# Kernel tuning notes

Measured on AMD Instinct MI355X. Metric: run time of the kernel, lower is better.

Reference implementation:

```python
import jax, jax.numpy as jnp
import numpy as np

BS, C, H, W = 2, 128, 80, 160
P, G = 9, 8
GC = C // G
EPS = 1e-5


def _layernorm_c(x, g, b):
    # x: (bs, C, H, W); LayerNorm over channel dim (to_3d dim=2 -> norm over c)
    m = jnp.mean(x, axis=1, keepdims=True)
    v = jnp.mean((x - m) ** 2, axis=1, keepdims=True)
    return (x - m) / jnp.sqrt(v + EPS) * g[None, :, None, None] + b[None, :, None, None]


def _conv1x1(x, w, b):
    return jnp.einsum('bchw,oc->bohw', x, w) + b[None, :, None, None]


def _bilinear_sample(feat, pts):
    # feat (bs,C,H,W); pts (bs,N,2) normalized [0,1]; zero padding outside (DAF convention)
    bs, c, h, w = feat.shape
    x = pts[..., 0] * w - 0.5
    y = pts[..., 1] * h - 0.5
    x0 = jnp.floor(x)
    y0 = jnp.floor(y)
    dx = x - x0
    dy = y - y0
    x0i = x0.astype(jnp.int32)
    y0i = y0.astype(jnp.int32)

    def corner(xi, yi, wgt):
        valid = (xi >= 0) & (xi < w) & (yi >= 0) & (yi < h)
        xc = jnp.clip(xi, 0, w - 1)
        yc = jnp.clip(yi, 0, h - 1)
        g = jax.vmap(lambda f, yy, xx: f[:, yy, xx].T)(feat, yc, xc)  # (bs,N,C)
        return g * (wgt * valid)[..., None]

    return (corner(x0i, y0i, (1 - dx) * (1 - dy))
            + corner(x0i + 1, y0i, dx * (1 - dy))
            + corner(x0i, y0i + 1, (1 - dx) * dy)
            + corner(x0i + 1, y0i + 1, dx * dy))


def _branch(match_flat, anchor, feat_value, wmap, kp_w, kp_b):
    bs = feat_value.shape[0]
    hw = H * W
    # Sparse1DKeyPointsGenerator: learned 1D offsets along the disparity (x) direction
    off = match_flat @ kp_w.T + kp_b  # (bs, HW, P)
    anc = anchor.reshape(bs, hw, P, 2)
    kp = jnp.stack([anc[..., 0] + off, anc[..., 1]], axis=-1)  # (bs,HW,P,2)
    # group-softmax attention weights over num_pts
    wts = wmap.transpose(0, 2, 3, 1).reshape(bs, hw, P, G)  # channel c = p*G + g
    wts = jax.nn.softmax(wts, axis=2)
    # deformable aggregation: bilinear gather at key points + group-weighted sum over pts
    sampled = _bilinear_sample(feat_value, kp.reshape(bs, hw * P, 2))
    sampled = sampled.reshape(bs, hw, P, G, GC)
    out = jnp.einsum('bnpgc,bnpg->bngc', sampled, wts).reshape(bs, hw, C)
    out = out.reshape(bs, H, W, C).transpose(0, 3, 1, 2)
    return out, kp


def _forward(mask, match, context, geometric, context_anchor_points, geometric_anchor_points,
             ln_g, ln_b, lnc_g, lnc_b, lng_g, lng_b,
             wc_w, wc_b, wg_w, wg_b, vc_w, vc_b, vg_w, vg_b,
             out_w, out_b, kpc_w, kpc_b, kpg_w, kpg_b):
    bs = match.shape[0]
    hw = H * W
    match_n = _layernorm_c(match, ln_g, ln_b)
    context_n = _layernorm_c(context, lnc_g, lnc_b)
    geometric_n = _layernorm_c(geometric, lng_g, lng_b)
    ctx_val = _conv1x1(context_n, vc_w, vc_b)
    geo_val = _conv1x1(geometric_n, vg_w, vg_b)
    match_flat = match_n.reshape(bs, C, hw).transpose(0, 2, 1)  # (bs,HW,C)
    wc = _conv1x1(match_n, wc_w, wc_b)  # (bs,G*P,H,W)
    wg = _conv1x1(match_n, wg_w, wg_b)
    ctx_out, ctx_kp = _branch(match_flat, context_anchor_points, ctx_val, wc, kpc_w, kpc_b)
    geo_out, geo_kp = _branch(match_flat, geometric_anchor_points, geo_val, wg, kpg_w, kpg_b)
    out = jnp.concatenate([ctx_out * mask, geo_out], axis=1)
    out = _conv1x1(out, out_w, out_b)  # proj_drop is identity (p=0)
    return out, ctx_kp.reshape(bs, H, W, P, 2), geo_kp.reshape(bs, H, W, P, 2)


def setup_inputs() -> dict:
    key = jax.random.key(0)
    ks = jax.random.split(key, 20)

    def wn(k, shape):
        return jax.random.normal(k, shape, jnp.float32) * 0.02

    return {
        'mask': jax.random.uniform(ks[0], (BS, 1, H, W), jnp.float32),
        'match': jax.random.normal(ks[1], (BS, C, H, W), jnp.float32),
        'context': jax.random.normal(ks[2], (BS, C, H, W), jnp.float32),
        'geometric': jax.random.normal(ks[3], (BS, C, H, W), jnp.float32),
        'context_anchor_points': jax.random.uniform(ks[4], (BS, H, W, P, 2), jnp.float32),
        'geometric_anchor_points': jax.random.uniform(ks[5], (BS, H, W, P, 2), jnp.float32),
        'ln_g': jnp.ones((C,), jnp.float32), 'ln_b': jnp.zeros((C,), jnp.float32),
        'lnc_g': jnp.ones((C,), jnp.float32), 'lnc_b': jnp.zeros((C,), jnp.float32),
        'lng_g': jnp.ones((C,), jnp.float32), 'lng_b': jnp.zeros((C,), jnp.float32),
        'wc_w': wn(ks[6], (G * P, C)), 'wc_b': jnp.zeros((G * P,), jnp.float32),
        'wg_w': wn(ks[7], (G * P, C)), 'wg_b': jnp.zeros((G * P,), jnp.float32),
        'vc_w': wn(ks[8], (C, C)), 'vc_b': jnp.zeros((C,), jnp.float32),
        'vg_w': wn(ks[9], (C, C)), 'vg_b': jnp.zeros((C,), jnp.float32),
        'out_w': wn(ks[10], (C, 2 * C)), 'out_b': jnp.zeros((C,), jnp.float32),
        'kpc_w': wn(ks[11], (P, C)), 'kpc_b': jnp.zeros((P,), jnp.float32),
        'kpg_w': wn(ks[12], (P, C)), 'kpg_b': jnp.zeros((P,), jnp.float32),
    }


def reference(mask, match, context, geometric, context_anchor_points, geometric_anchor_points,
              ln_g, ln_b, lnc_g, lnc_b, lng_g, lng_b,
              wc_w, wc_b, wg_w, wg_b, vc_w, vc_b, vg_w, vg_b,
              out_w, out_b, kpc_w, kpc_b, kpg_w, kpg_b):
    return _forward(mask, match, context, geometric, context_anchor_points, geometric_anchor_points,
                    ln_g, ln_b, lnc_g, lnc_b, lng_g, lng_b,
                    wc_w, wc_b, wg_w, wg_b, vc_w, vc_b, vg_w, vg_b,
                    out_w, out_b, kpc_w, kpc_b, kpg_w, kpg_b)
```

## Files before the change

### kernel.cpp

```cpp
#include <hip/hip_runtime.h>
#include <hip/hip_bf16.h>

typedef __hip_bfloat16 bf16;
typedef __bf16 b16x8 __attribute__((ext_vector_type(8)));
typedef float f32x4 __attribute__((ext_vector_type(4)));
typedef float f32x2 __attribute__((ext_vector_type(2)));

#define HWs   12800
#define NPIX  25600
#define IMG_H 80
#define IMG_W 160

#define OFF_VCB  0
#define OFF_VGB  16384
#define OFF_MATB 32768
#define OFF_OUTB 53504
#define NW_BF16  86272

static __device__ inline unsigned char enc_fp8(float v)
{
    return (unsigned char)(__builtin_amdgcn_cvt_pk_fp8_f32(v, v, 0, false) & 0xFF);
}

__global__ __launch_bounds__(256) void k_prep(
    const float* __restrict__ vc_w, const float* __restrict__ vg_w,
    const float* __restrict__ wc_w, const float* __restrict__ wg_w,
    const float* __restrict__ kpc_w, const float* __restrict__ kpg_w,
    const float* __restrict__ out_w,
    const float* __restrict__ wc_b, const float* __restrict__ wg_b,
    const float* __restrict__ kpc_b, const float* __restrict__ kpg_b,
    bf16* __restrict__ wbuf, float* __restrict__ bias176)
{
    int i = blockIdx.x * 256 + threadIdx.x;
    if (i < 16384) {
        wbuf[i] = __float2bfloat16(vc_w[i]);
    } else if (i < 32768) {
        wbuf[i] = __float2bfloat16(vg_w[i - 16384]);
    } else if (i < 53504) {
        int j = i - 32768; int row = j >> 7; int c = j & 127;
        float v;
        if (row < 72)       v = wc_w[row * 128 + c];
        else if (row < 144) v = wg_w[(row - 72) * 128 + c];
        else if (row < 153) v = kpc_w[(row - 144) * 128 + c];
        else                v = kpg_w[(row - 153) * 128 + c];
        wbuf[i] = __float2bfloat16(v);
    } else if (i < NW_BF16) {
        wbuf[i] = __float2bfloat16(out_w[i - 53504]);
    } else if (i < NW_BF16 + 176) {
        int j = i - NW_BF16;
        float v = 0.f;
        if (j < 72)       v = wc_b[j];
        else if (j < 144) v = wg_b[j - 72];
        else if (j < 153) v = kpc_b[j - 144];
        else if (j < 162) v = kpg_b[j - 153];
        bias176[j] = v;
    }
}

__global__ __launch_bounds__(256) void k_stage1(
    const float* __restrict__ match, const float* __restrict__ context, const float* __restrict__ geometric,
    const float* __restrict__ ln_g, const float* __restrict__ ln_b,
    const float* __restrict__ lnc_g, const float* __restrict__ lnc_b,
    const float* __restrict__ lng_g, const float* __restrict__ lng_b,
    const float* __restrict__ vc_b, const float* __restrict__ vg_b,
    const bf16* __restrict__ wbuf, const float* __restrict__ bias176,
    const float* __restrict__ anc_c, const float* __restrict__ anc_g,
    unsigned char* __restrict__ ctx8, unsigned char* __restrict__ geo8,
    bf16* __restrict__ wts_g, float* __restrict__ coords_g,
    float* __restrict__ kp_out)
{
    __shared__ __align__(16) bf16 tile_s[32 * 136];
    __shared__ bf16 logit_s[32 * 144];
    __shared__ float offs_s[32 * 18];
    __shared__ float red1[8][32];
    __shared__ float red2[8][32];

    int bx = blockIdx.x;
    int seg = bx / 800;
    int tile = bx - seg * 800;
    int t = threadIdx.x;
    int pixbase = tile * 32;

    const float* X  = (seg == 0) ? context : (seg == 1) ? geometric : match;
    const float* gg = (seg == 0) ? lnc_g   : (seg == 1) ? lng_g     : ln_g;
    const float* bb = (seg == 0) ? lnc_b   : (seg == 1) ? lng_b     : ln_b;

    int p = t & 31;
    int cq = t >> 5;
    int b = pixbase >= HWs;
    int hw = pixbase - b * HWs;
    const float* base = X + ((size_t)b * 128) * HWs + hw + p;
    float xv[16];
#pragma unroll
    for (int j = 0; j < 16; j++) xv[j] = base[(size_t)(cq * 16 + j) * HWs];

    int wv = t >> 6;
    int lane = t & 63;
    int s = wv >> 1;
    int h = wv & 1;
    int lrow = lane & 15;
    int lq = lane >> 4;
    const bf16* Wb = (seg == 0) ? wbuf + OFF_VCB
                   : (seg == 1) ? wbuf + OFF_VGB
                                : wbuf + OFF_MATB;
    b16x8 wf[4][4];
    float bpre[4];
#pragma unroll
    for (int i = 0; i < 4; i++) {
        int o = (h + 2 * i) * 16 + lrow;
        const bf16* wr = Wb + (size_t)o * 128;
#pragma unroll
        for (int kk = 0; kk < 4; kk++)
            wf[i][kk] = *(const b16x8*)(wr + (kk * 4 + lq) * 8);
        bpre[i] = (seg == 0) ? vc_b[o] : (seg == 1) ? vg_b[o] : bias176[o];
    }

    {
        float s1 = 0.f, s2 = 0.f;
#pragma unroll
        for (int j = 0; j < 16; j++) { s1 += xv[j]; s2 += xv[j] * xv[j]; }
        red1[cq][p] = s1; red2[cq][p] = s2;
        __syncthreads();
        float S1 = 0.f, S2 = 0.f;
#pragma unroll
        for (int q = 0; q < 8; q++) { S1 += red1[q][p]; S2 += red2[q][p]; }
        float mean = S1 * (1.f / 128.f);
        float var  = fmaxf(S2 * (1.f / 128.f) - mean * mean, 0.f);
        float rstd = rsqrtf(var + 1e-5f);
#pragma unroll
        for (int j = 0; j < 16; j++) {
            int c = cq * 16 + j;
            float y = (xv[j] - mean) * rstd * gg[c] + bb[c];
            tile_s[p * 136 + c] = __float2bfloat16(y);
        }
        __syncthreads();
    }

    const b16x8* arow = (const b16x8*)(tile_s + (s * 16 + lrow) * 136);
    b16x8 af[4];
#pragma unroll
    for (int kk = 0; kk < 4; kk++) af[kk] = arow[kk * 4 + lq];

    if (seg < 2) {
        unsigned char* val = (seg == 0) ? ctx8 : geo8;
#pragma unroll
        for (int i = 0; i < 4; i++) {
            int o = (h + 2 * i) * 16 + lrow;
            f32x4 acc = {0.f, 0.f, 0.f, 0.f};
#pragma unroll
            for (int kk = 0; kk < 4; kk++)
                acc = __builtin_amdgcn_mfma_f32_16x16x32_bf16(af[kk], wf[i][kk], acc, 0, 0, 0);
#pragma unroll
            for (int r = 0; r < 4; r++) {
                int pix = pixbase + s * 16 + lq * 4 + r;
                val[(size_t)pix * 128 + o] = enc_fp8(acc[r] + bpre[i]);
            }
        }
        return;
    }

#pragma unroll
    for (int i = 0; i < 4; i++) {
        int o = (h + 2 * i) * 16 + lrow;
        f32x4 acc = {0.f, 0.f, 0.f, 0.f};
#pragma unroll
        for (int kk = 0; kk < 4; kk++)
            acc = __builtin_amdgcn_mfma_f32_16x16x32_bf16(af[kk], wf[i][kk], acc, 0, 0, 0);
#pragma unroll
        for (int r = 0; r < 4; r++) {
            int row = s * 16 + lq * 4 + r;
            logit_s[row * 144 + o] = __float2bfloat16(acc[r] + bpre[i]);
        }
    }
    for (int ot = h + 8; ot < 11; ot += 2) {
        int o = ot * 16 + lrow;
        const bf16* wr = Wb + (size_t)o * 128;
        f32x4 acc = {0.f, 0.f, 0.f, 0.f};
#pragma unroll
        for (int kk = 0; kk < 4; kk++)
            acc = __builtin_amdgcn_mfma_f32_16x16x32_bf16(af[kk], *(const b16x8*)(wr + (kk * 4 + lq) * 8), acc, 0, 0, 0);
        float bias = bias176[o];
#pragma unroll
        for (int r = 0; r < 4; r++) {
            int row = s * 16 + lq * 4 + r;
            float v = acc[r] + bias;
            if (o < 144)       logit_s[row * 144 + o] = __float2bfloat16(v);
            else if (o < 162)  offs_s[row * 18 + (o - 144)] = v;
        }
    }
    __syncthreads();

#pragma unroll
    for (int i = 0; i < 2; i++) {
        int task = t + 256 * i;
        int lp = task >> 4;
        int sub = task & 15;
        int br = sub >> 3;
        int g = sub & 7;
        const bf16* basel = logit_s + lp * 144 + br * 72 + g;
        float v[9];
        float m = -1e30f;
#pragma unroll
        for (int pp = 0; pp < 9; pp++) { v[pp] = __bfloat162float(basel[pp * 8]); m = fmaxf(m, v[pp]); }
        float ssum = 0.f;
#pragma unroll
        for (int pp = 0; pp < 9; pp++) { v[pp] = __expf(v[pp] - m); ssum += v[pp]; }
        float inv = 1.f / ssum;
        int pix = pixbase + lp;
        bf16* wbp = wts_g + ((size_t)pix * 2 + br) * 72 + g * 9;
#pragma unroll
        for (int pp = 0; pp < 9; pp++) wbp[pp] = __float2bfloat16(v[pp] * inv);
    }

    for (int i = 0; i < 3; i++) {
        int task = t + 256 * i;
        if (task < 576) {
            int lp = task / 18;
            int sub = task - lp * 18;
            int br = sub / 9;
            int pp = sub - br * 9;
            int pix = pixbase + lp;
            float off = offs_s[lp * 18 + br * 9 + pp];
            const float* anc = br ? anc_g : anc_c;
            float ax = anc[(size_t)pix * 18 + pp * 2];
            float ay = anc[(size_t)pix * 18 + pp * 2 + 1];
            float kx = ax + off;
            float* kpo = kp_out + (size_t)br * (NPIX * 18) + (size_t)pix * 18 + pp * 2;
            kpo[0] = kx;
            kpo[1] = ay;
            float* cbp = coords_g + ((size_t)pix * 2 + br) * 18 + pp * 2;
            cbp[0] = kx * 160.f - 0.5f;
            cbp[1] = ay * 80.f - 0.5f;
        }
    }
}

__global__ __launch_bounds__(256) void k_agg(
    const unsigned char* __restrict__ ctx8, const unsigned char* __restrict__ geo8,
    const bf16* __restrict__ wts_g, const float* __restrict__ coords_g,
    const float* __restrict__ mask,
    bf16* __restrict__ aggf)
{
    int t = threadIdx.x;
    int wv = t >> 6;
    int lane = t & 63;
    int q = lane >> 4;
    int sub = lane & 15;
    int c0 = sub * 8;
    int g = sub >> 1;

    int bx = blockIdx.x;
    int xcd = bx & 7;
    int br = xcd >> 2;
    int grp = (bx >> 3) * 4 + (xcd & 3);
    int pix = grp * 16 + wv * 4 + q;
    int tk = pix * 2 + br;
    int b = pix >= HWs;
    int rowbase = b * HWs;

    const unsigned char* val = br ? geo8 : ctx8;
    const float* cb = coords_g + (size_t)tk * 18;
    const bf16* wb = wts_g + (size_t)tk * 72 + g * 9;

    float wtv[9];
#pragma unroll
    for (int pp = 0; pp < 9; pp++) wtv[pp] = __bfloat162float(wb[pp]);

    float acc[8] = {0.f, 0.f, 0.f, 0.f, 0.f, 0.f, 0.f, 0.f};
    for (int pp = 0; pp < 9; pp++) {
        float px = cb[pp * 2];
        float py = cb[pp * 2 + 1];
        float fx = floorf(px), fy = floorf(py);
        float dx = px - fx, dy = py - fy;
        int x0 = (int)fx, y0 = (int)fy;
        float wt = wtv[pp];
#pragma unroll
        for (int c4 = 0; c4 < 4; c4++) {
            int xi = x0 + (c4 & 1);
            int yi = y0 + (c4 >> 1);
            bool ok = (xi >= 0) & (xi < IMG_W) & (yi >= 0) & (yi < IMG_H);
            int xc = min(max(xi, 0), IMG_W - 1);
            int yc = min(max(yi, 0), IMG_H - 1);
            float wx = (c4 & 1) ? dx : 1.f - dx;
            float wy = (c4 >> 1) ? dy : 1.f - dy;
            float wgt = ok ? wx * wy * wt : 0.f;
            uint2 u = *(const uint2*)(val + (size_t)(rowbase + yc * IMG_W + xc) * 128 + c0);
            f32x2 v01 = __builtin_amdgcn_cvt_pk_f32_fp8(u.x, false);
            f32x2 v23 = __builtin_amdgcn_cvt_pk_f32_fp8(u.x, true);
            f32x2 v45 = __builtin_amdgcn_cvt_pk_f32_fp8(u.y, false);
            f32x2 v67 = __builtin_amdgcn_cvt_pk_f32_fp8(u.y, true);
            acc[0] += wgt * v01[0]; acc[1] += wgt * v01[1];
            acc[2] += wgt * v23[0]; acc[3] += wgt * v23[1];
            acc[4] += wgt * v45[0]; acc[5] += wgt * v45[1];
            acc[6] += wgt * v67[0]; acc[7] += wgt * v67[1];
        }
    }
    float mv = (br == 0) ? mask[pix] : 1.f;
    b16x8 pk;
#pragma unroll
    for (int j = 0; j < 8; j++) pk[j] = (__bf16)(acc[j] * mv);
    *(b16x8*)(aggf + (size_t)pix * 256 + br * 128 + c0) = pk;
}

__global__ __launch_bounds__(256) void k_out(
    const bf16* __restrict__ aggf,
    const bf16* __restrict__ outb, const float* __restrict__ out_b,
    float* __restrict__ out)
{
    int t = threadIdx.x;
    int pixbase = blockIdx.x * 32;
    int wv = t >> 6;
    int lane = t & 63;
    int s = wv >> 1;
    int h = wv & 1;
    int lrow = lane & 15;
    int lq = lane >> 4;
    const b16x8* arow = (const b16x8*)(aggf + (size_t)(pixbase + s * 16 + lrow) * 256);
    b16x8 af[8];
#pragma unroll
    for (int kk = 0; kk < 8; kk++) af[kk] = arow[kk * 4 + lq];
    int b = pixbase >= HWs;
#pragma unroll
    for (int i = 0; i < 4; i++) {
        int o = (h + 2 * i) * 16 + lrow;
        const bf16* wrow = outb + (size_t)o * 256;
        f32x4 acc = {0.f, 0.f, 0.f, 0.f};
#pragma unroll
        for (int kk = 0; kk < 8; kk++)
            acc = __builtin_amdgcn_mfma_f32_16x16x32_bf16(af[kk], *(const b16x8*)(wrow + (kk * 4 + lq) * 8), acc, 0, 0, 0);
        float bias = out_b[o];
#pragma unroll
        for (int r = 0; r < 4; r++) {
            int pix = pixbase + s * 16 + lq * 4 + r;
            int hw = pix - b * HWs;
            out[(size_t)b * (128 * HWs) + (size_t)o * HWs + hw] = acc[r] + bias;
        }
    }
}

extern "C" void kernel_launch(void* const* d_in, const int* in_sizes, int n_in,
                              void* d_out, int out_size, void* d_ws, size_t ws_size,
                              hipStream_t stream)
{
    const float* mask      = (const float*)d_in[0];
    const float* match     = (const float*)d_in[1];
    const float* context   = (const float*)d_in[2];
    const float* geometric = (const float*)d_in[3];
    const float* anc_c     = (const float*)d_in[4];
    const float* anc_g     = (const float*)d_in[5];
    const float* ln_g  = (const float*)d_in[6];
    const float* ln_b  = (const float*)d_in[7];
    const float* lnc_g = (const float*)d_in[8];
    const float* lnc_b = (const float*)d_in[9];
    const float* lng_g = (const float*)d_in[10];
    const float* lng_b = (const float*)d_in[11];
    const float* wc_w  = (const float*)d_in[12];
    const float* wc_b  = (const float*)d_in[13];
    const float* wg_w  = (const float*)d_in[14];
    const float* wg_b  = (const float*)d_in[15];
    const float* vc_w  = (const float*)d_in[16];
    const float* vc_b  = (const float*)d_in[17];
    const float* vg_w  = (const float*)d_in[18];
    const float* vg_b  = (const float*)d_in[19];
    const float* out_w = (const float*)d_in[20];
    const float* out_b = (const float*)d_in[21];
    const float* kpc_w = (const float*)d_in[22];
    const float* kpc_b = (const float*)d_in[23];
    const float* kpg_w = (const float*)d_in[24];
    const float* kpg_b = (const float*)d_in[25];

    char* w = (char*)d_ws;
    unsigned char* ctx8 = (unsigned char*)(w);
    unsigned char* geo8 = (unsigned char*)(w + 3276800);
    bf16*  wts_g    = (bf16*)(w + 6553600);
    float* coords_g = (float*)(w + 13926400);
    bf16*  aggf     = (bf16*)(w + 17612800);
    bf16*  wbuf     = (bf16*)(w + 30720000);
    float* bias176  = (float*)(w + 30892544);

    float* outp = (float*)d_out;
    float* kp_out = outp + (size_t)2 * 128 * HWs;

    k_prep<<<(NW_BF16 + 176 + 255) / 256, 256, 0, stream>>>(
        vc_w, vg_w, wc_w, wg_w, kpc_w, kpg_w, out_w,
        wc_b, wg_b, kpc_b, kpg_b, wbuf, bias176);
    k_stage1<<<2400, 256, 0, stream>>>(match, context, geometric,
                                       ln_g, ln_b, lnc_g, lnc_b, lng_g, lng_b,
                                       vc_b, vg_b, wbuf, bias176,
                                       anc_c, anc_g,
                                       ctx8, geo8, wts_g, coords_g, kp_out);
    k_agg<<<3200, 256, 0, stream>>>(ctx8, geo8, wts_g, coords_g, mask, aggf);
    k_out<<<800, 256, 0, stream>>>(aggf, wbuf + OFF_OUTB, out_b, outp);
}
```

Baseline: 202.3 us.

## Fuse aggregation with output projection and transpose MFMA for vectorized stores

Merges the deformable aggregation and output 1x1 projection into one kernel so the aggregated features stay in shared memory instead of round-tripping through a global bf16 buffer, and drops one launch. Stage 1 swaps the MFMA operand order so each lane holds four consecutive output channels. This lets the fp8 value stores, bf16 logit stores and kp/coord writes become packed vector stores. It also interleaves segment assignment across blocks. In exchange, each fused block handles both branches for 16 pixels serially, which may lower parallelism in the gather phase.

```diff
diff --git a/kernel.cpp b/kernel.cpp
--- a/kernel.cpp
+++ b/kernel.cpp
@@ -3,6 +3,7 @@
 
 typedef __hip_bfloat16 bf16;
 typedef __bf16 b16x8 __attribute__((ext_vector_type(8)));
+typedef __bf16 b16x4 __attribute__((ext_vector_type(4)));
 typedef float f32x4 __attribute__((ext_vector_type(4)));
 typedef float f32x2 __attribute__((ext_vector_type(2)));
 
@@ -16,11 +17,6 @@
 #define OFF_MATB 32768
 #define OFF_OUTB 53504
 #define NW_BF16  86272
-
-static __device__ inline unsigned char enc_fp8(float v)
-{
-    return (unsigned char)(__builtin_amdgcn_cvt_pk_fp8_f32(v, v, 0, false) & 0xFF);
-}
 
 __global__ __launch_bounds__(256) void k_prep(
     const float* __restrict__ vc_w, const float* __restrict__ vg_w,
@@ -70,14 +66,14 @@
     float* __restrict__ kp_out)
 {
     __shared__ __align__(16) bf16 tile_s[32 * 136];
-    __shared__ bf16 logit_s[32 * 144];
+    __shared__ __align__(16) bf16 logit_s[32 * 148];
     __shared__ float offs_s[32 * 18];
     __shared__ float red1[8][32];
     __shared__ float red2[8][32];
 
     int bx = blockIdx.x;
-    int seg = bx / 800;
-    int tile = bx - seg * 800;
+    int seg = bx % 3;
+    int tile = bx / 3;
     int t = threadIdx.x;
     int pixbase = tile * 32;
 
@@ -104,7 +100,6 @@
                    : (seg == 1) ? wbuf + OFF_VGB
                                 : wbuf + OFF_MATB;
     b16x8 wf[4][4];
-    float bpre[4];
 #pragma unroll
     for (int i = 0; i < 4; i++) {
         int o = (h + 2 * i) * 16 + lrow;
@@ -112,7 +107,6 @@
 #pragma unroll
         for (int kk = 0; kk < 4; kk++)
             wf[i][kk] = *(const b16x8*)(wr + (kk * 4 + lq) * 8);
-        bpre[i] = (seg == 0) ? vc_b[o] : (seg == 1) ? vg_b[o] : bias176[o];
     }
 
     {
@@ -141,51 +135,62 @@
 #pragma unroll
     for (int kk = 0; kk < 4; kk++) af[kk] = arow[kk * 4 + lq];
 
+    int prow = s * 16 + lrow;
+
     if (seg < 2) {
         unsigned char* val = (seg == 0) ? ctx8 : geo8;
+        const float* vb = (seg == 0) ? vc_b : vg_b;
+        size_t prix = (size_t)(pixbase + prow) * 128;
 #pragma unroll
         for (int i = 0; i < 4; i++) {
-            int o = (h + 2 * i) * 16 + lrow;
+            int obase = (h + 2 * i) * 16 + lq * 4;
             f32x4 acc = {0.f, 0.f, 0.f, 0.f};
 #pragma unroll
             for (int kk = 0; kk < 4; kk++)
-                acc = __builtin_amdgcn_mfma_f32_16x16x32_bf16(af[kk], wf[i][kk], acc, 0, 0, 0);
-#pragma unroll
-            for (int r = 0; r < 4; r++) {
-                int pix = pixbase + s * 16 + lq * 4 + r;
-                val[(size_t)pix * 128 + o] = enc_fp8(acc[r] + bpre[i]);
+                acc = __builtin_amdgcn_mfma_f32_16x16x32_bf16(wf[i][kk], af[kk], acc, 0, 0, 0);
+            f32x4 bv = *(const f32x4*)(vb + obase);
+            int u = __builtin_amdgcn_cvt_pk_fp8_f32(acc[0] + bv[0], acc[1] + bv[1], 0, false);
+            u = __builtin_amdgcn_cvt_pk_fp8_f32(acc[2] + bv[2], acc[3] + bv[3], u, true);
+            *(unsigned int*)(val + prix + obase) = (unsigned int)u;
+        }
+        return;
+    }
+
+#pragma unroll
+    for (int i = 0; i < 4; i++) {
+        int obase = (h + 2 * i) * 16 + lq * 4;
+        f32x4 acc = {0.f, 0.f, 0.f, 0.f};
+#pragma unroll
+        for (int kk = 0; kk < 4; kk++)
+            acc = __builtin_amdgcn_mfma_f32_16x16x32_bf16(wf[i][kk], af[kk], acc, 0, 0, 0);
+        f32x4 bv = *(const f32x4*)(bias176 + obase);
+        b16x4 pk4;
+#pragma unroll
+        for (int r = 0; r < 4; r++) pk4[r] = (__bf16)(acc[r] + bv[r]);
+        *(b16x4*)(logit_s + prow * 148 + obase) = pk4;
+    }
+    for (int ot = h + 8; ot < 11; ot += 2) {
+        int obase = ot * 16 + lq * 4;
+        const bf16* wr = Wb + (size_t)(ot * 16 + lrow) * 128;
+        f32x4 acc = {0.f, 0.f, 0.f, 0.f};
+#pragma unroll
+        for (int kk = 0; kk < 4; kk++)
+            acc = __builtin_amdgcn_mfma_f32_16x16x32_bf16(*(const b16x8*)(wr + (kk * 4 + lq) * 8), af[kk], acc, 0, 0, 0);
+        f32x4 bv = *(const f32x4*)(bias176 + obase);
+        if (ot == 8) {
+            b16x4 pk4;
+#pragma unroll
+            for (int r = 0; r < 4; r++) pk4[r] = (__bf16)(acc[r] + bv[r]);
+            *(b16x4*)(logit_s + prow * 148 + obase) = pk4;
+        } else if (ot == 9) {
+#pragma unroll
+            for (int r = 0; r < 4; r++)
+                offs_s[prow * 18 + (obase - 144) + r] = acc[r] + bv[r];
+        } else {
+            if (lq == 0) {
+                offs_s[prow * 18 + 16] = acc[0] + bv[0];
+                offs_s[prow * 18 + 17] = acc[1] + bv[1];
             }
-        }
-        return;
-    }
-
-#pragma unroll
-    for (int i = 0; i < 4; i++) {
-        int o = (h + 2 * i) * 16 + lrow;
-        f32x4 acc = {0.f, 0.f, 0.f, 0.f};
-#pragma unroll
-        for (int kk = 0; kk < 4; kk++)
-            acc = __builtin_amdgcn_mfma_f32_16x16x32_bf16(af[kk], wf[i][kk], acc, 0, 0, 0);
-#pragma unroll
-        for (int r = 0; r < 4; r++) {
-            int row = s * 16 + lq * 4 + r;
-            logit_s[row * 144 + o] = __float2bfloat16(acc[r] + bpre[i]);
-        }
-    }
-    for (int ot = h + 8; ot < 11; ot += 2) {
-        int o = ot * 16 + lrow;
-        const bf16* wr = Wb + (size_t)o * 128;
-        f32x4 acc = {0.f, 0.f, 0.f, 0.f};
-#pragma unroll
-        for (int kk = 0; kk < 4; kk++)
-            acc = __builtin_amdgcn_mfma_f32_16x16x32_bf16(af[kk], *(const b16x8*)(wr + (kk * 4 + lq) * 8), acc, 0, 0, 0);
-        float bias = bias176[o];
-#pragma unroll
-        for (int r = 0; r < 4; r++) {
-            int row = s * 16 + lq * 4 + r;
-            float v = acc[r] + bias;
-            if (o < 144)       logit_s[row * 144 + o] = __float2bfloat16(v);
-            else if (o < 162)  offs_s[row * 18 + (o - 144)] = v;
         }
     }
     __syncthreads();
@@ -197,7 +202,7 @@
         int sub = task & 15;
         int br = sub >> 3;
         int g = sub & 7;
-        const bf16* basel = logit_s + lp * 144 + br * 72 + g;
+        const bf16* basel = logit_s + lp * 148 + br * 72 + g;
         float v[9];
         float m = -1e30f;
 #pragma unroll
@@ -216,31 +221,31 @@
         int task = t + 256 * i;
         if (task < 576) {
             int lp = task / 18;
-            int sub = task - lp * 18;
-            int br = sub / 9;
-            int pp = sub - br * 9;
+            int sub2 = task - lp * 18;
+            int br = sub2 / 9;
+            int pp = sub2 - br * 9;
             int pix = pixbase + lp;
             float off = offs_s[lp * 18 + br * 9 + pp];
             const float* anc = br ? anc_g : anc_c;
-            float ax = anc[(size_t)pix * 18 + pp * 2];
-            float ay = anc[(size_t)pix * 18 + pp * 2 + 1];
-            float kx = ax + off;
-            float* kpo = kp_out + (size_t)br * (NPIX * 18) + (size_t)pix * 18 + pp * 2;
-            kpo[0] = kx;
-            kpo[1] = ay;
-            float* cbp = coords_g + ((size_t)pix * 2 + br) * 18 + pp * 2;
-            cbp[0] = kx * 160.f - 0.5f;
-            cbp[1] = ay * 80.f - 0.5f;
+            f32x2 a2 = *(const f32x2*)(anc + (size_t)pix * 18 + pp * 2);
+            float kx = a2[0] + off;
+            f32x2 kp2 = {kx, a2[1]};
+            *(f32x2*)(kp_out + (size_t)br * (NPIX * 18) + (size_t)pix * 18 + pp * 2) = kp2;
+            f32x2 c2 = {kx * 160.f - 0.5f, a2[1] * 80.f - 0.5f};
+            *(f32x2*)(coords_g + ((size_t)pix * 2 + br) * 18 + pp * 2) = c2;
         }
     }
 }
 
-__global__ __launch_bounds__(256) void k_agg(
+__global__ __launch_bounds__(256) void k_fuse(
     const unsigned char* __restrict__ ctx8, const unsigned char* __restrict__ geo8,
     const bf16* __restrict__ wts_g, const float* __restrict__ coords_g,
     const float* __restrict__ mask,
-    bf16* __restrict__ aggf)
+    const bf16* __restrict__ outb, const float* __restrict__ out_b,
+    float* __restrict__ out)
 {
+    __shared__ __align__(16) bf16 agg_s[16 * 264];
+
     int t = threadIdx.x;
     int wv = t >> 6;
     int lane = t & 63;
@@ -249,92 +254,79 @@
     int c0 = sub * 8;
     int g = sub >> 1;
 
-    int bx = blockIdx.x;
-    int xcd = bx & 7;
-    int br = xcd >> 2;
-    int grp = (bx >> 3) * 4 + (xcd & 3);
-    int pix = grp * 16 + wv * 4 + q;
-    int tk = pix * 2 + br;
-    int b = pix >= HWs;
+    int pixbase = blockIdx.x * 16;
+    int qw = wv * 4 + q;
+    int pix = pixbase + qw;
+    int b = pixbase >= HWs;
     int rowbase = b * HWs;
 
-    const unsigned char* val = br ? geo8 : ctx8;
-    const float* cb = coords_g + (size_t)tk * 18;
-    const bf16* wb = wts_g + (size_t)tk * 72 + g * 9;
-
-    float wtv[9];
-#pragma unroll
-    for (int pp = 0; pp < 9; pp++) wtv[pp] = __bfloat162float(wb[pp]);
-
-    float acc[8] = {0.f, 0.f, 0.f, 0.f, 0.f, 0.f, 0.f, 0.f};
-    for (int pp = 0; pp < 9; pp++) {
-        float px = cb[pp * 2];
-        float py = cb[pp * 2 + 1];
-        float fx = floorf(px), fy = floorf(py);
-        float dx = px - fx, dy = py - fy;
-        int x0 = (int)fx, y0 = (int)fy;
-        float wt = wtv[pp];
-#pragma unroll
-        for (int c4 = 0; c4 < 4; c4++) {
-            int xi = x0 + (c4 & 1);
-            int yi = y0 + (c4 >> 1);
-            bool ok = (xi >= 0) & (xi < IMG_W) & (yi >= 0) & (yi < IMG_H);
-            int xc = min(max(xi, 0), IMG_W - 1);
-            int yc = min(max(yi, 0), IMG_H - 1);
-            float wx = (c4 & 1) ? dx : 1.f - dx;
-            float wy = (c4 >> 1) ? dy : 1.f - dy;
-            float wgt = ok ? wx * wy * wt : 0.f;
-            uint2 u = *(const uint2*)(val + (size_t)(rowbase + yc * IMG_W + xc) * 128 + c0);
-            f32x2 v01 = __builtin_amdgcn_cvt_pk_f32_fp8(u.x, false);
-            f32x2 v23 = __builtin_amdgcn_cvt_pk_f32_fp8(u.x, true);
-            f32x2 v45 = __builtin_amdgcn_cvt_pk_f32_fp8(u.y, false);
-            f32x2 v67 = __builtin_amdgcn_cvt_pk_f32_fp8(u.y, true);
-            acc[0] += wgt * v01[0]; acc[1] += wgt * v01[1];
-            acc[2] += wgt * v23[0]; acc[3] += wgt * v23[1];
-            acc[4] += wgt * v45[0]; acc[5] += wgt * v45[1];
-            acc[6] += wgt * v67[0]; acc[7] += wgt * v67[1];
-        }
-    }
-    float mv = (br == 0) ? mask[pix] : 1.f;
-    b16x8 pk;
-#pragma unroll
-    for (int j = 0; j < 8; j++) pk[j] = (__bf16)(acc[j] * mv);
-    *(b16x8*)(aggf + (size_t)pix * 256 + br * 128 + c0) = pk;
-}
-
-__global__ __launch_bounds__(256) void k_out(
-    const bf16* __restrict__ aggf,
-    const bf16* __restrict__ outb, const float* __restrict__ out_b,
-    float* __restrict__ out)
-{
-    int t = threadIdx.x;
-    int pixbase = blockIdx.x * 32;
-    int wv = t >> 6;
-    int lane = t & 63;
-    int s = wv >> 1;
-    int h = wv & 1;
+#pragma unroll
+    for (int br = 0; br < 2; br++) {
+        const unsigned char* val = br ? geo8 : ctx8;
+        int tk = pix * 2 + br;
+        const float* cb = coords_g + (size_t)tk * 18;
+        const bf16* wb = wts_g + (size_t)tk * 72 + g * 9;
+
+        float wtv[9];
+#pragma unroll
+        for (int pp = 0; pp < 9; pp++) wtv[pp] = __bfloat162float(wb[pp]);
+
+        float acc[8] = {0.f, 0.f, 0.f, 0.f, 0.f, 0.f, 0.f, 0.f};
+        for (int pp = 0; pp < 9; pp++) {
+            f32x2 cc = *(const f32x2*)(cb + pp * 2);
+            float fx = floorf(cc[0]), fy = floorf(cc[1]);
+            float dx = cc[0] - fx, dy = cc[1] - fy;
+            int x0 = (int)fx, y0 = (int)fy;
+            float wt = wtv[pp];
+#pragma unroll
+            for (int c4 = 0; c4 < 4; c4++) {
+                int xi = x0 + (c4 & 1);
+                int yi = y0 + (c4 >> 1);
+                bool ok = (xi >= 0) & (xi < IMG_W) & (yi >= 0) & (yi < IMG_H);
+                int xc = min(max(xi, 0), IMG_W - 1);
+                int yc = min(max(yi, 0), IMG_H - 1);
+                float wx = (c4 & 1) ? dx : 1.f - dx;
+                float wy = (c4 >> 1) ? dy : 1.f - dy;
+                float wgt = ok ? wx * wy * wt : 0.f;
+                uint2 u = *(const uint2*)(val + (size_t)(rowbase + yc * IMG_W + xc) * 128 + c0);
+                f32x2 v01 = __builtin_amdgcn_cvt_pk_f32_fp8(u.x, false);
+                f32x2 v23 = __builtin_amdgcn_cvt_pk_f32_fp8(u.x, true);
+                f32x2 v45 = __builtin_amdgcn_cvt_pk_f32_fp8(u.y, false);
+                f32x2 v67 = __builtin_amdgcn_cvt_pk_f32_fp8(u.y, true);
+                acc[0] += wgt * v01[0]; acc[1] += wgt * v01[1];
+                acc[2] += wgt * v23[0]; acc[3] += wgt * v23[1];
+                acc[4] += wgt * v45[0]; acc[5] += wgt * v45[1];
+                acc[6] += wgt * v67[0]; acc[7] += wgt * v67[1];
+            }
+        }
+        float mv = (br == 0) ? mask[pix] : 1.f;
+        b16x8 pk;
+#pragma unroll
+        for (int j = 0; j < 8; j++) pk[j] = (__bf16)(acc[j] * mv);
+        *(b16x8*)(agg_s + qw * 264 + br * 128 + c0) = pk;
+    }
+    __syncthreads();
+
     int lrow = lane & 15;
     int lq = lane >> 4;
-    const b16x8* arow = (const b16x8*)(aggf + (size_t)(pixbase + s * 16 + lrow) * 256);
     b16x8 af[8];
 #pragma unroll
-    for (int kk = 0; kk < 8; kk++) af[kk] = arow[kk * 4 + lq];
-    int b = pixbase >= HWs;
-#pragma unroll
-    for (int i = 0; i < 4; i++) {
-        int o = (h + 2 * i) * 16 + lrow;
+    for (int kk = 0; kk < 8; kk++)
+        af[kk] = *(const b16x8*)(agg_s + lrow * 264 + (kk * 4 + lq) * 8);
+#pragma unroll
+    for (int i = 0; i < 2; i++) {
+        int o = (wv + 4 * i) * 16 + lrow;
         const bf16* wrow = outb + (size_t)o * 256;
         f32x4 acc = {0.f, 0.f, 0.f, 0.f};
 #pragma unroll
         for (int kk = 0; kk < 8; kk++)
             acc = __builtin_amdgcn_mfma_f32_16x16x32_bf16(af[kk], *(const b16x8*)(wrow + (kk * 4 + lq) * 8), acc, 0, 0, 0);
         float bias = out_b[o];
-#pragma unroll
-        for (int r = 0; r < 4; r++) {
-            int pix = pixbase + s * 16 + lq * 4 + r;
-            int hw = pix - b * HWs;
-            out[(size_t)b * (128 * HWs) + (size_t)o * HWs + hw] = acc[r] + bias;
-        }
+        f32x4 st;
+#pragma unroll
+        for (int r = 0; r < 4; r++) st[r] = acc[r] + bias;
+        int hw0 = pixbase + lq * 4 - rowbase;
+        *(f32x4*)(out + (size_t)b * (128 * HWs) + (size_t)o * HWs + hw0) = st;
     }
 }
 
@@ -374,7 +366,6 @@
     unsigned char* geo8 = (unsigned char*)(w + 3276800);
     bf16*  wts_g    = (bf16*)(w + 6553600);
     float* coords_g = (float*)(w + 13926400);
-    bf16*  aggf     = (bf16*)(w + 17612800);
     bf16*  wbuf     = (bf16*)(w + 30720000);
     float* bias176  = (float*)(w + 30892544);
 
@@ -389,6 +380,6 @@
                                        vc_b, vg_b, wbuf, bias176,
                                        anc_c, anc_g,
                                        ctx8, geo8, wts_g, coords_g, kp_out);
-    k_agg<<<3200, 256, 0, stream>>>(ctx8, geo8, wts_g, coords_g, mask, aggf);
-    k_out<<<800, 256, 0, stream>>>(aggf, wbuf + OFF_OUTB, out_b, outp);
+    k_fuse<<<1600, 256, 0, stream>>>(ctx8, geo8, wts_g, coords_g, mask,
+                                     wbuf + OFF_OUTB, out_b, outp);
 }
```

New measurement: 199.1 us. No clear change (-1.6%).
